# Kernel tuning notes

Measured on AMD Instinct MI355X. Metric: run time of the kernel, lower is better.

Reference implementation:

```python
import jax, jax.numpy as jnp
import numpy as np
from jax import lax

DN = ('NCHW', 'OIHW', 'NCHW')  # torch conv layout
QMIN, QMAX = -128.0, 127.0     # qint8 range


def setup_inputs() -> dict:
    key = jax.random.key(0)
    k1, k2, k3, k4 = jax.random.split(key, 4)
    B, Cin, Cout, H, W, K = 8, 320, 320, 64, 64, 3
    x = jax.random.normal(k1, (B, Cin, H, W), dtype=jnp.float32)
    # int8 weight values stored as int32 (int_repr of per-channel quantized weight)
    weight_int = jax.random.randint(k2, (Cout, Cin, K, K), -128, 128, dtype=jnp.int32)
    weight_scales = jax.random.uniform(k3, (Cout,), jnp.float32, 0.001, 0.01)
    act_scales = jnp.float32(0.04)        # per-tensor activation scale
    act_zero_points = jnp.float32(3.0)    # per-tensor activation zero point
    act_scales_inv = 1.0 / act_scales
    bias = jax.random.normal(k4, (Cout,), dtype=jnp.float32) * 0.1
    # precomputed buffers (from_float): padding>0 path
    weight_sum_by_input_channels = weight_int.astype(jnp.float32).sum(axis=1, keepdims=True)  # [O,1,K,K]
    scale = weight_scales * act_scales  # fused dequant scale per output channel
    return {
        'x': x,
        'weight_int': weight_int,
        'weight_sum_by_input_channels': weight_sum_by_input_channels,
        'scale': scale,
        'act_scales_inv': act_scales_inv,
        'act_zero_points': act_zero_points,
        'bias': bias,
    }


def reference(x, weight_int, weight_sum_by_input_channels, scale,
              act_scales_inv, act_zero_points, bias):
    stride, pad = 1, 1
    # per-tensor activation quantization: x_int = clamp(round(x/s) + zp)
    x_int = jnp.clip(jnp.round(x * act_scales_inv) + act_zero_points, QMIN, QMAX)
    w = weight_int.astype(jnp.float32)
    # integer conv (emulated in f32): conv(x_int, W_int)
    acc = lax.conv_general_dilated(x_int, w, (stride, stride),
                                   [(pad, pad), (pad, pad)], dimension_numbers=DN)
    # zero-point correction: zp * conv(ones, sum_i W_int) (spatially varying near padding)
    ones = jnp.ones_like(x[:, :1])  # [B,1,H,W]
    corr = lax.conv_general_dilated(ones, weight_sum_by_input_channels, (stride, stride),
                                    [(pad, pad), (pad, pad)], dimension_numbers=DN)
    corr = corr * act_zero_points
    # dequant: per-output-channel scale = w_scale * a_scale, plus float bias
    out = scale[None, :, None, None] * (acc - corr) + bias[None, :, None, None]
    return out
```

## Files before the change

kernel.cpp:

```cpp
#include <hip/hip_runtime.h>
#include <hip/hip_bf16.h>


typedef int v4i __attribute__((ext_vector_type(4)));

typedef const unsigned int __attribute__((address_space(1)))* gas_uptr;
typedef unsigned int __attribute__((address_space(3)))* las_uptr;

#define B_   8
#define CIN  320
#define COUT 320
#define H_   64
#define W_   64
#define HW_  4096
#define HP   66
#define WP   66
#define XPAD_BYTES (B_*HP*WP*CIN)
#define W8_BYTES (COUT*9*CIN)

__global__ __launch_bounds__(256) void repack_bias_kernel(const int* __restrict__ wint,
                                                          unsigned char* __restrict__ w8,
                                                          const float* __restrict__ wsum,
                                                          const float* __restrict__ scale,
                                                          const float* __restrict__ bias,
                                                          const float* __restrict__ zp_p,
                                                          float* __restrict__ be) {
    int j = blockIdx.x * 256 + threadIdx.x;
    if (j < COUT) {
        float s = 0.f;
        #pragma unroll
        for (int tp = 0; tp < 9; ++tp) s += wsum[j*9 + tp];
        be[j] = bias[j] - scale[j] * zp_p[0] * s;
    }
    int co  = j / 720;
    int r   = j - co * 720;
    int tap = r / 80;
    int d   = r - tap * 80;
    int ci  = d * 4;
    const int* base = wint + (co * CIN + ci) * 9 + tap;
    unsigned b0 = (unsigned)(base[0]  & 0xFF);
    unsigned b1 = (unsigned)(base[9]  & 0xFF);
    unsigned b2 = (unsigned)(base[18] & 0xFF);
    unsigned b3 = (unsigned)(base[27] & 0xFF);
    ((unsigned*)w8)[j] = b0 | (b1 << 8) | (b2 << 16) | (b3 << 24);
}

__global__ __launch_bounds__(256) void quant_pad_kernel(const float* __restrict__ x,
                                                        unsigned char* __restrict__ xpad,
                                                        const float* __restrict__ inv_p,
                                                        const float* __restrict__ zp_p) {
    __shared__ __align__(16) unsigned lds[64 * 81];
    int bid = blockIdx.x;
    int b  = bid / HP;
    int ph = bid - b * HP;
    int t  = threadIdx.x;
    float inv = inv_p[0];
    float zp  = zp_p[0];
    int zpi = (int)rintf(zp);
    unsigned zd = ((unsigned)(zpi & 0xFF)) * 0x01010101u;

    unsigned* rowbase = (unsigned*)(xpad + (size_t)((b * HP + ph) * WP) * CIN);

    if (ph == 0 || ph == HP - 1) {
        for (int j = t; j < WP * CIN / 4; j += 256) rowbase[j] = zd;
        return;
    }
    int h = ph - 1;
    const float* xrow = x + (size_t)b * CIN * H_ * W_ + h * W_;
    int wq = t & 15;
    int cg = t >> 4;
    #pragma unroll
    for (int i = 0; i < 5; ++i) {
        int ci0 = i * 64 + cg * 4;
        float4 f[4];
        #pragma unroll
        for (int jj = 0; jj < 4; ++jj)
            f[jj] = *(const float4*)(xrow + (size_t)(ci0 + jj) * HW_ + wq * 4);
        #pragma unroll
        for (int k = 0; k < 4; ++k) {
            unsigned d = 0;
            #pragma unroll
            for (int jj = 0; jj < 4; ++jj) {
                float v = (&f[jj].x)[k];
                float q = rintf(v * inv) + zp;
                q = fminf(fmaxf(q, -128.0f), 127.0f);
                int qi = (int)q;
                d |= ((unsigned)(qi & 0xFF)) << (8 * jj);
            }
            lds[(wq * 4 + k) * 81 + (ci0 >> 2)] = d;
        }
    }
    __syncthreads();
    if (t < 80)            rowbase[t] = zd;
    else if (t < 160)      rowbase[65 * 80 + (t - 80)] = zd;
    for (int j = t; j < 64 * 80; j += 256) {
        int p = j / 80;
        int d = j - p * 80;
        rowbase[80 + j] = lds[p * 81 + d];
    }
}

__global__ __launch_bounds__(256, 2) void conv_gemm_kernel(const unsigned char* __restrict__ xpad,
                                                           const unsigned char* __restrict__ w8,
                                                           const float* __restrict__ scale,
                                                           const float* __restrict__ be,
                                                           float* __restrict__ out) {
    __shared__ __align__(16) unsigned char Al[5 * 128 * 64];

    int t    = threadIdx.x;
    int lane = t & 63;
    int wave = t >> 6;
    int wm   = wave & 1;
    int wn   = wave >> 1;
    int m0   = blockIdx.x * 128;
    int n0   = blockIdx.y * 160;

    int p  = t >> 2;
    int qs = (t & 3) ^ ((p >> 1) & 3);
    int pix0 = m0 + p;
    int pix1 = pix0 + 64;
    int b0i = pix0 >> 12, hw0 = pix0 & 4095;
    int b1i = pix1 >> 12, hw1 = pix1 & 4095;
    const unsigned char* ap0 = xpad + (size_t)(((b0i * HP + (hw0 >> 6)) * WP + (hw0 & 63)) * CIN) + qs * 16;
    const unsigned char* ap1 = xpad + (size_t)(((b1i * HP + (hw1 >> 6)) * WP + (hw1 & 63)) * CIN) + qs * 16;

    int colc = lane & 15;
    int q    = lane >> 4;
    int aAddr[4];
    #pragma unroll
    for (int mi = 0; mi < 4; ++mi) {
        int P = wm * 64 + mi * 16 + colc;
        aAddr[mi] = P * 64 + ((q ^ ((P >> 1) & 3)) * 16);
    }

    const unsigned char* bptr[5];
    #pragma unroll
    for (int ni = 0; ni < 5; ++ni) {
        int co = n0 + wn * 80 + ni * 16 + colc;
        bptr[ni] = w8 + (size_t)co * (9 * CIN) + q * 16;
    }

    v4i acc[4][5];
    v4i zero = {0, 0, 0, 0};
    #pragma unroll
    for (int mi = 0; mi < 4; ++mi)
        #pragma unroll
        for (int ni = 0; ni < 5; ++ni) acc[mi][ni] = zero;

    #pragma unroll 1
    for (int kh = 0; kh < 3; ++kh) {
        #pragma unroll 1
        for (int kw = 0; kw < 3; ++kw) {
            int aoff = (kh * WP + kw) * CIN;
            int boff = (kh * 3 + kw) * CIN;

            v4i bf[5][5];
            #pragma unroll
            for (int c5 = 0; c5 < 5; ++c5)
                #pragma unroll
                for (int ni = 0; ni < 5; ++ni)
                    bf[c5][ni] = *(const v4i*)(bptr[ni] + boff + c5 * 64);

            #pragma unroll
            for (int c5 = 0; c5 < 5; ++c5) {
                __builtin_amdgcn_global_load_lds((gas_uptr)(const void*)(ap0 + aoff + c5 * 64),
                                                 (las_uptr)(Al + c5 * 8192 + t * 16), 16, 0, 0);
                __builtin_amdgcn_global_load_lds((gas_uptr)(const void*)(ap1 + aoff + c5 * 64),
                                                 (las_uptr)(Al + c5 * 8192 + 4096 + t * 16), 16, 0, 0);
            }
            __syncthreads();

            #pragma unroll
            for (int c5 = 0; c5 < 5; ++c5) {
                v4i a[4];
                #pragma unroll
                for (int mi = 0; mi < 4; ++mi)
                    a[mi] = *(const v4i*)(Al + c5 * 8192 + aAddr[mi]);
                #pragma unroll
                for (int mi = 0; mi < 4; ++mi)
                    #pragma unroll
                    for (int ni = 0; ni < 5; ++ni)
                        acc[mi][ni] = __builtin_amdgcn_mfma_i32_16x16x64_i8(a[mi], bf[c5][ni], acc[mi][ni], 0, 0, 0);
            }
            __syncthreads();
        }
    }

    #pragma unroll
    for (int ni = 0; ni < 5; ++ni) {
        int co = n0 + wn * 80 + ni * 16 + colc;
        float s  = scale[co];
        float bz = be[co];
        #pragma unroll
        for (int mi = 0; mi < 4; ++mi) {
            int pix = m0 + wm * 64 + mi * 16 + q * 4;
            int bb2 = pix >> 12;
            int hw  = pix & 4095;
            v4i v = acc[mi][ni];
            float4 o;
            o.x = s * (float)v.x + bz;
            o.y = s * (float)v.y + bz;
            o.z = s * (float)v.z + bz;
            o.w = s * (float)v.w + bz;
            *(float4*)(out + (size_t)(bb2 * COUT + co) * HW_ + hw) = o;
        }
    }
}

extern "C" void kernel_launch(void* const* d_in, const int* in_sizes, int n_in,
                              void* d_out, int out_size, void* d_ws, size_t ws_size,
                              hipStream_t stream) {
    const float* x     = (const float*)d_in[0];
    const int*   wint  = (const int*)d_in[1];
    const float* wsum  = (const float*)d_in[2];
    const float* scale = (const float*)d_in[3];
    const float* inv_p = (const float*)d_in[4];
    const float* zp_p  = (const float*)d_in[5];
    const float* bias  = (const float*)d_in[6];
    float* out = (float*)d_out;

    unsigned char* xpad = (unsigned char*)d_ws;
    unsigned char* w8   = xpad + XPAD_BYTES;
    float*         be   = (float*)(w8 + W8_BYTES);

    repack_bias_kernel<<<(COUT * 720) / 256, 256, 0, stream>>>(wint, w8, wsum, scale, bias, zp_p, be);
    quant_pad_kernel<<<B_ * HP, 256, 0, stream>>>(x, xpad, inv_p, zp_p);

    dim3 grid((B_ * H_ * W_) / 128, COUT / 160);
    conv_gemm_kernel<<<grid, 256, 0, stream>>>(xpad, w8, scale, be, out);
}
```

Before: 161.3 us.

## Replace LDS-staged block tile with single-wave tiles loading A directly from global

The conv GEMM kernel moves from 256-thread blocks that stage the activation tile in LDS via global_load_lds with barriers to 64-thread single-wave blocks that load both A and B fragments straight from global memory into registers. The inner kw loop is now fully unrolled and the pointers advance per kh row. This removes LDS traffic and block-wide synchronisation. In exchange, activation rows are no longer shared across waves, so global and L2 traffic rises, and the launch uses many more, smaller blocks.

```diff
diff --git a/kernel.cpp b/kernel.cpp
--- a/kernel.cpp
+++ b/kernel.cpp
@@ -3,9 +3,6 @@
 
 
 typedef int v4i __attribute__((ext_vector_type(4)));
-
-typedef const unsigned int __attribute__((address_space(1)))* gas_uptr;
-typedef unsigned int __attribute__((address_space(3)))* las_uptr;
 
 #define B_   8
 #define CIN  320
@@ -100,44 +97,30 @@
     }
 }
 
-__global__ __launch_bounds__(256, 2) void conv_gemm_kernel(const unsigned char* __restrict__ xpad,
-                                                           const unsigned char* __restrict__ w8,
-                                                           const float* __restrict__ scale,
-                                                           const float* __restrict__ be,
-                                                           float* __restrict__ out) {
-    __shared__ __align__(16) unsigned char Al[5 * 128 * 64];
-
-    int t    = threadIdx.x;
-    int lane = t & 63;
-    int wave = t >> 6;
-    int wm   = wave & 1;
-    int wn   = wave >> 1;
-    int m0   = blockIdx.x * 128;
-    int n0   = blockIdx.y * 160;
-
-    int p  = t >> 2;
-    int qs = (t & 3) ^ ((p >> 1) & 3);
-    int pix0 = m0 + p;
-    int pix1 = pix0 + 64;
-    int b0i = pix0 >> 12, hw0 = pix0 & 4095;
-    int b1i = pix1 >> 12, hw1 = pix1 & 4095;
-    const unsigned char* ap0 = xpad + (size_t)(((b0i * HP + (hw0 >> 6)) * WP + (hw0 & 63)) * CIN) + qs * 16;
-    const unsigned char* ap1 = xpad + (size_t)(((b1i * HP + (hw1 >> 6)) * WP + (hw1 & 63)) * CIN) + qs * 16;
-
+__global__ __launch_bounds__(64) void conv_gemm_kernel(const unsigned char* __restrict__ xpad,
+                                                       const unsigned char* __restrict__ w8,
+                                                       const float* __restrict__ scale,
+                                                       const float* __restrict__ be,
+                                                       float* __restrict__ out) {
+    int lane = threadIdx.x;
     int colc = lane & 15;
     int q    = lane >> 4;
-    int aAddr[4];
+    int m0   = blockIdx.x * 64;
+    int n0   = blockIdx.y * 80;
+
+    const unsigned char* ap[4];
     #pragma unroll
     for (int mi = 0; mi < 4; ++mi) {
-        int P = wm * 64 + mi * 16 + colc;
-        aAddr[mi] = P * 64 + ((q ^ ((P >> 1) & 3)) * 16);
-    }
-
-    const unsigned char* bptr[5];
+        int pix = m0 + mi * 16 + colc;
+        int bb  = pix >> 12;
+        int hw  = pix & 4095;
+        ap[mi] = xpad + (size_t)(((bb * HP + (hw >> 6)) * WP + (hw & 63)) * CIN) + q * 16;
+    }
+    const unsigned char* bp[5];
     #pragma unroll
     for (int ni = 0; ni < 5; ++ni) {
-        int co = n0 + wn * 80 + ni * 16 + colc;
-        bptr[ni] = w8 + (size_t)co * (9 * CIN) + q * 16;
+        int co = n0 + ni * 16 + colc;
+        bp[ni] = w8 + (size_t)co * (9 * CIN) + q * 16;
     }
 
     v4i acc[4][5];
@@ -149,51 +132,39 @@
 
     #pragma unroll 1
     for (int kh = 0; kh < 3; ++kh) {
-        #pragma unroll 1
+        #pragma unroll
         for (int kw = 0; kw < 3; ++kw) {
-            int aoff = (kh * WP + kw) * CIN;
-            int boff = (kh * 3 + kw) * CIN;
-
-            v4i bf[5][5];
             #pragma unroll
-            for (int c5 = 0; c5 < 5; ++c5)
+            for (int c5 = 0; c5 < 5; ++c5) {
+                int off = kw * CIN + c5 * 64;
+                v4i a[4], b[5];
+                #pragma unroll
+                for (int mi = 0; mi < 4; ++mi)
+                    a[mi] = *(const v4i*)(ap[mi] + off);
                 #pragma unroll
                 for (int ni = 0; ni < 5; ++ni)
-                    bf[c5][ni] = *(const v4i*)(bptr[ni] + boff + c5 * 64);
-
-            #pragma unroll
-            for (int c5 = 0; c5 < 5; ++c5) {
-                __builtin_amdgcn_global_load_lds((gas_uptr)(const void*)(ap0 + aoff + c5 * 64),
-                                                 (las_uptr)(Al + c5 * 8192 + t * 16), 16, 0, 0);
-                __builtin_amdgcn_global_load_lds((gas_uptr)(const void*)(ap1 + aoff + c5 * 64),
-                                                 (las_uptr)(Al + c5 * 8192 + 4096 + t * 16), 16, 0, 0);
-            }
-            __syncthreads();
-
-            #pragma unroll
-            for (int c5 = 0; c5 < 5; ++c5) {
-                v4i a[4];
-                #pragma unroll
-                for (int mi = 0; mi < 4; ++mi)
-                    a[mi] = *(const v4i*)(Al + c5 * 8192 + aAddr[mi]);
+                    b[ni] = *(const v4i*)(bp[ni] + off);
                 #pragma unroll
                 for (int mi = 0; mi < 4; ++mi)
                     #pragma unroll
                     for (int ni = 0; ni < 5; ++ni)
-                        acc[mi][ni] = __builtin_amdgcn_mfma_i32_16x16x64_i8(a[mi], bf[c5][ni], acc[mi][ni], 0, 0, 0);
+                        acc[mi][ni] = __builtin_amdgcn_mfma_i32_16x16x64_i8(a[mi], b[ni], acc[mi][ni], 0, 0, 0);
             }
-            __syncthreads();
         }
+        #pragma unroll
+        for (int mi = 0; mi < 4; ++mi) ap[mi] += WP * CIN;
+        #pragma unroll
+        for (int ni = 0; ni < 5; ++ni) bp[ni] += 3 * CIN;
     }
 
     #pragma unroll
     for (int ni = 0; ni < 5; ++ni) {
-        int co = n0 + wn * 80 + ni * 16 + colc;
+        int co = n0 + ni * 16 + colc;
         float s  = scale[co];
         float bz = be[co];
         #pragma unroll
         for (int mi = 0; mi < 4; ++mi) {
-            int pix = m0 + wm * 64 + mi * 16 + q * 4;
+            int pix = m0 + mi * 16 + q * 4;
             int bb2 = pix >> 12;
             int hw  = pix & 4095;
             v4i v = acc[mi][ni];
@@ -226,6 +197,6 @@
     repack_bias_kernel<<<(COUT * 720) / 256, 256, 0, stream>>>(wint, w8, wsum, scale, bias, zp_p, be);
     quant_pad_kernel<<<B_ * HP, 256, 0, stream>>>(x, xpad, inv_p, zp_p);
 
-    dim3 grid((B_ * H_ * W_) / 128, COUT / 160);
-    conv_gemm_kernel<<<grid, 256, 0, stream>>>(xpad, w8, scale, be, out);
-}
+    dim3 grid((B_ * H_ * W_) / 64, COUT / 80);
+    conv_gemm_kernel<<<grid, 64, 0, stream>>>(xpad, w8, scale, be, out);
+}
```

Result: slower. 168.0 us (+4.2%).
